# Kernel tuning notes

Hardware: AMD Instinct MI355X
Metric: run time of the kernel (lower is better)

The kernel has to match this reference:

```python
import jax, jax.numpy as jnp
import numpy as np

B = 1024      # batch
H = 512       # n_hidden
F = 32        # lstm_features
CIN = 4       # input channels
K = 30        # conv kernel
STRIDE = 6
L = 924       # input length -> T = (924-30)//6+1 = 150
KD = 40       # deconv kernel
NSTEPS = 10   # lstm_future_out
DN = ('NCH', 'OIH', 'NCH')


def setup_inputs() -> dict:
    key = jax.random.key(0)
    ks = jax.random.split(key, 14)
    s = 0.05
    rn = lambda k, shape: jax.random.normal(k, shape, jnp.float32) * s
    return dict(
        x=jax.random.normal(ks[0], (B, CIN, L), jnp.float32),
        conv_w=rn(ks[1], (F, CIN, K)), conv_b=rn(ks[2], (F,)),
        Wih0=rn(ks[3], (4 * H, F)), Whh0=rn(ks[4], (4 * H, H)),
        bih0=rn(ks[5], (4 * H,)), bhh0=rn(ks[6], (4 * H,)),
        Wih1=rn(ks[7], (4 * H, H)), Whh1=rn(ks[8], (4 * H, H)),
        bih1=rn(ks[9], (4 * H,)), bhh1=rn(ks[10], (4 * H,)),
        dec_w=rn(ks[11], (F, H)), dec_b=rn(ks[12], (F,)),
        deconv_w=rn(ks[13], (F, 1, KD)),
    )


def _cell(x, h, c, Wih, Whh, b):
    # PyTorch LSTM gate order: i, f, g, o
    g = x @ Wih.T + h @ Whh.T + b
    i, f, gg, o = jnp.split(g, 4, axis=-1)
    c = jax.nn.sigmoid(f) * c + jax.nn.sigmoid(i) * jnp.tanh(gg)
    h = jax.nn.sigmoid(o) * jnp.tanh(c)
    return h, c


def _lstm_layer(seq, Wih, Whh, b):
    # seq: [T, B, in] -> ys: [T, B, H], final (h, c)
    n = seq.shape[1]
    h0 = jnp.zeros((n, H), seq.dtype)
    c0 = jnp.zeros((n, H), seq.dtype)
    def step(carry, x):
        h, c = _cell(x, carry[0], carry[1], Wih, Whh, b)
        return (h, c), h
    (hT, cT), ys = jax.lax.scan(step, (h0, c0), seq)
    return ys, hT, cT


def _forward(x, conv_w, conv_b, Wih0, Whh0, bih0, bhh0,
             Wih1, Whh1, bih1, bhh1, dec_w, dec_b, deconv_w):
    # encoder conv: [B,4,L] -> [B,F,T]
    z = jax.lax.conv_general_dilated(x, conv_w, (STRIDE,), [(0, 0)],
                                     dimension_numbers=DN) + conv_b[None, :, None]
    z = jax.nn.relu(z)
    seq = jnp.transpose(z, (2, 0, 1))  # [T, B, F]
    b0, b1 = bih0 + bhh0, bih1 + bhh1
    s0, h0, c0 = _lstm_layer(seq, Wih0, Whh0, b0)
    s1, h1, c1 = _lstm_layer(s0, Wih1, Whh1, b1)
    out = s1 @ dec_w.T + dec_b                 # [T, B, F]
    y0 = out[-1]                               # output[-2:-1] of encoder -> last decoded step
    def dec_step(carry, _):
        y, ha, ca, hb, cb = carry
        ha, ca = _cell(y, ha, ca, Wih0, Whh0, b0)
        hb, cb = _cell(ha, hb, cb, Wih1, Whh1, b1)
        y = hb @ dec_w.T + dec_b
        return (y, ha, ca, hb, cb), y
    _, fut = jax.lax.scan(dec_step, (y0, h0, c0, h1, c1), None, length=NSTEPS)
    fut = jnp.transpose(fut, (1, 2, 0))        # [B, F, 10]
    # ConvTranspose1d (stride=1, pad=0, no bias) == cross-correlation with
    # spatially flipped, channel-swapped kernel on input padded by KD-1.
    kt = jnp.transpose(jnp.flip(deconv_w, -1), (1, 0, 2))  # [1, F, KD]
    return jax.lax.conv_general_dilated(fut, kt, (1,), [(KD - 1, KD - 1)],
                                        dimension_numbers=DN)  # [B, 1, 49]


def reference(x, conv_w, conv_b, Wih0, Whh0, bih0, bhh0,
              Wih1, Whh1, bih1, bhh1, dec_w, dec_b, deconv_w):
    return _forward(x, conv_w, conv_b, Wih0, Whh0, bih0, bhh0,
                    Wih1, Whh1, bih1, bhh1, dec_w, dec_b, deconv_w)
```

## Files before the change

### kernel.cpp

```cpp
#include <hip/hip_runtime.h>
#include <hip/hip_bf16.h>

typedef __hip_bfloat16 bf16;
typedef __attribute__((ext_vector_type(8))) short short8;
typedef __attribute__((ext_vector_type(4))) float float4v;

#define B_    1024
#define H_    512
#define G4H   2048
#define F_    32
#define CIN_  4
#define K_    30
#define STRIDE_ 6
#define L_    924
#define T_    150
#define KD_   40
#define NSTEPS_ 10
#define BH    (B_ * H_)
#define STRF  16

__device__ __forceinline__ float sigmoidf_(float x) { return 1.f / (1.f + __expf(-x)); }
__device__ __forceinline__ float tanhf_(float x)    { return 1.f - 2.f / (__expf(2.f * x) + 1.f); }
__device__ __forceinline__ float b2f_(short s) {
    return __uint_as_float(((unsigned)(unsigned short)s) << 16);
}
__device__ __forceinline__ unsigned short f2bu_(float v) {
    union { __hip_bfloat16 b; unsigned short u; } cv;
    cv.b = __float2bfloat16(v);
    return cv.u;
}
__device__ __forceinline__ void stwt_(bf16* p, float v) {
    __hip_atomic_store((unsigned short*)p, f2bu_(v), __ATOMIC_RELAXED, __HIP_MEMORY_SCOPE_AGENT);
}

__global__ __launch_bounds__(256) void cvt_kernel(const float* __restrict__ src,
                                                  bf16* __restrict__ dst, int n) {
    int i = blockIdx.x * 256 + threadIdx.x;
    if (i < n) dst[i] = __float2bfloat16(src[i]);
}

__global__ void bias_kernel(const float* __restrict__ bih0, const float* __restrict__ bhh0,
                            const float* __restrict__ bih1, const float* __restrict__ bhh1,
                            float* __restrict__ b0, float* __restrict__ b1) {
    int i = blockIdx.x * 256 + threadIdx.x;
    if (i < G4H)      b0[i] = bih0[i] + bhh0[i];
    else if (i < 2*G4H) { int j = i - G4H; b1[j] = bih1[j] + bhh1[j]; }
}

__global__ __launch_bounds__(256) void conv_kernel(
    const float* __restrict__ x, const float* __restrict__ w,
    const float* __restrict__ cb, bf16* __restrict__ seq)
{
    __shared__ float w_lds[CIN_ * K_ * F_];
    __shared__ float x_lds[CIN_ * L_];
    int tid = threadIdx.x;
    int b = blockIdx.x;
    for (int i = tid; i < CIN_ * K_ * F_; i += 256) {
        int f = i & 31, r = i >> 5;
        w_lds[r * 32 + f] = w[f * (CIN_ * K_) + r];
    }
    const float* xb = x + (size_t)b * (CIN_ * L_);
    for (int i = tid; i < CIN_ * L_; i += 256)
        x_lds[i] = xb[i];
    __syncthreads();
    int f = tid & 31, tt = tid >> 5;
    float cbf = cb[f];
    for (int t0 = 0; t0 < T_; t0 += 8) {
        int t = t0 + tt;
        if (t < T_) {
            float acc = cbf;
            #pragma unroll
            for (int c = 0; c < CIN_; ++c) {
                const float* xr = x_lds + c * L_ + t * STRIDE_;
                const float* wr = w_lds + c * K_ * 32 + f;
                #pragma unroll
                for (int k = 0; k < K_; ++k)
                    acc += xr[k] * wr[k * 32];
            }
            acc = fmaxf(acc, 0.f);
            seq[(size_t)t * (B_ * F_) + b * F_ + f] = __float2bfloat16(acc);
        }
    }
}

__device__ __forceinline__ void wait2(const int* fa, int ta, const int* fb, int tb) {
    const int t = threadIdx.x;
    if (t < 64) {
        const int* p = nullptr; int tgt = 0;
        if (t < 32) { if (fa) { p = fa + t * STRF;        tgt = ta; } }
        else        { if (fb) { p = fb + (t - 32) * STRF; tgt = tb; } }
        for (;;) {
            int v = p ? __hip_atomic_load(p, __ATOMIC_RELAXED, __HIP_MEMORY_SCOPE_AGENT)
                      : 0x7fffffff;
            if (__all(v >= tgt)) break;
            __builtin_amdgcn_s_sleep(2);
        }
    }
    __syncthreads();
    __builtin_amdgcn_fence(__ATOMIC_ACQUIRE, "agent");
}

__device__ __forceinline__ void signal1(int* f, int val) {
    __syncthreads();
    if (threadIdx.x == 0) {
        __builtin_amdgcn_s_waitcnt(0);
        __hip_atomic_store(f, val, __ATOMIC_RELAXED, __HIP_MEMORY_SCOPE_AGENT);
    }
}

template<int P1KS, int XSTR, typename MW>
__device__ __forceinline__ void layer_step(
    const bf16* __restrict__ X, const bf16* __restrict__ Hprev,
    const short8* __restrict__ WldsH, const short8* __restrict__ WldsI,
    float bi, float bff, float bg, float bo,
    float (&creg)[16], bf16* __restrict__ Hwt, bf16* __restrict__ Hloc,
    int m0, int j0, int wid, int lane, MW&& midwait)
{
    const int row16 = lane & 15;
    const int quad  = lane >> 4;
    const int mrow  = m0 + wid * 64 + row16;

    constexpr int TOT = 16 + P1KS;
    constexpr int NC  = (TOT + 3) / 4;

    const bf16* hb[4];
    const bf16* xb[4];
    #pragma unroll
    for (int q = 0; q < 4; ++q) {
        hb[q] = Hprev + (size_t)(mrow + q * 16) * H_ + quad * 8;
        xb[q] = X + (size_t)(mrow + q * 16) * XSTR + quad * 8;
    }

    float4v st[2][4][4];

    auto issue = [&](int c) {
        #pragma unroll
        for (int g = 0; g < 4; ++g) {
            int k = c * 4 + g;
            if (k < TOT) {
                #pragma unroll
                for (int q = 0; q < 4; ++q)
                    st[c & 1][g][q] = (k < 16)
                        ? *(const float4v*)(hb[q] + k * 32)
                        : *(const float4v*)(xb[q] + (k - 16) * 32);
            }
        }
        __builtin_amdgcn_sched_barrier(0);
    };
    auto ka = [&](int c) {
        #pragma unroll
        for (int g = 0; g < 4; ++g) {
            int k = c * 4 + g;
            if (k < TOT) {
                #pragma unroll
                for (int q = 0; q < 4; ++q)
                    asm volatile("" :: "v"(st[c & 1][g][q]));
            }
        }
    };

    issue(0);
    if (NC > 1) issue(1);
    midwait();

    float4v acc[4][4];
    #pragma unroll
    for (int q = 0; q < 4; ++q)
        #pragma unroll
        for (int g = 0; g < 4; ++g)
            acc[q][g] = (float4v){0.f, 0.f, 0.f, 0.f};

    #pragma unroll
    for (int c = 0; c < NC; ++c) {
        ka(c);
        #pragma unroll
        for (int g = 0; g < 4; ++g) {
            int k = c * 4 + g;
            if (k < TOT) {
                const short8* W = (k < 16) ? WldsH : WldsI;
                const int ks = (k < 16) ? k : (k - 16);
                short8 av[4];
                #pragma unroll
                for (int q = 0; q < 4; ++q)
                    av[q] = __builtin_bit_cast(short8, st[c & 1][g][q]);
                #pragma unroll
                for (int gg = 0; gg < 4; ++gg) {
                    short8 bfr = W[(ks * 4 + gg) * 64 + lane];
                    #pragma unroll
                    for (int q = 0; q < 4; ++q)
                        acc[q][gg] = __builtin_amdgcn_mfma_f32_16x16x32_bf16(av[q], bfr, acc[q][gg], 0, 0, 0);
                }
            }
        }
        if (c + 2 < NC) issue(c + 2);
    }

    float hval[16];
    #pragma unroll
    for (int ms = 0; ms < 4; ++ms) {
        #pragma unroll
        for (int r = 0; r < 4; ++r) {
            float ig = sigmoidf_(acc[ms][0][r] + bi);
            float fg = sigmoidf_(acc[ms][1][r] + bff);
            float gg = tanhf_(acc[ms][2][r] + bg);
            float og = sigmoidf_(acc[ms][3][r] + bo);
            float cn = fg * creg[ms * 4 + r] + ig * gg;
            creg[ms * 4 + r] = cn;
            hval[ms * 4 + r] = og * tanhf_(cn);
        }
    }

    unsigned wA[16];
    #pragma unroll
    for (int i = 0; i < 16; ++i) {
        float o = __shfl_xor(hval[i], 1);
        float lo = (lane & 1) ? o : hval[i];
        float hi = (lane & 1) ? hval[i] : o;
        wA[i] = (unsigned)f2bu_(lo) | ((unsigned)f2bu_(hi) << 16);
    }
    unsigned long long q[16];
    #pragma unroll
    for (int i = 0; i < 16; ++i) {
        unsigned o2 = __shfl_xor(wA[i], 2);
        q[i] = (lane & 2) ? (((unsigned long long)wA[i] << 32) | o2)
                          : (((unsigned long long)o2 << 32) | wA[i]);
    }
    const int cchunk = j0 + (row16 & ~3);
    #pragma unroll
    for (int i = 0; i < 16; ++i) {
        if ((i >> 2) == (lane & 3)) {
            int ms = i >> 2, r = i & 3;
            size_t off = (size_t)(m0 + wid * 64 + ms * 16 + quad * 4 + r) * H_ + cchunk;
            if (Hwt)
                __hip_atomic_store((unsigned long long*)(Hwt + off), q[i],
                                   __ATOMIC_RELAXED, __HIP_MEMORY_SCOPE_AGENT);
            if (Hloc)
                *(unsigned long long*)(Hloc + off) = q[i];
        }
    }
}

struct PP {
    const bf16 *seq, *Wih0, *Whh0, *Wih1, *Whh1, *dwb;
    const float *b0, *b1, *dec_b;
    float *fut;
    bf16 *h0, *h0loc, *h1, *y;
    int *flags;
};

__global__ __launch_bounds__(256, 1) void lstm_persist(PP P) {
    __shared__ short8 WldsH[4096];
    __shared__ short8 WldsI[4096];

    const int bid   = blockIdx.x;
    const int gsw   = bid & 7;
    const bool isL0 = (gsw < 4);
    const int mg    = gsw & 3;
    const int jj    = bid >> 3;
    const int lb    = mg * 32 + jj;
    const int j0    = jj * 16;
    const int m0    = mg * 256;
    const int tid   = threadIdx.x;
    const int wid   = tid >> 6;
    const int lane  = tid & 63;

    {
        const bf16* Whh = isL0 ? P.Whh0 : P.Whh1;
        for (int i = 0; i < 16; ++i) {
            int s = tid + i * 256;
            int frag = s >> 6, ln = s & 63;
            int ks = frag >> 2, g = frag & 3;
            WldsH[s] = *(const short8*)(Whh + (size_t)(g * H_ + j0 + (ln & 15)) * H_
                                        + ks * 32 + (ln >> 4) * 8);
        }
        if (isL0) {
            int frag = tid >> 6, ln = tid & 63;
            int g = frag & 3;
            WldsI[tid] = *(const short8*)(P.Wih0 + (size_t)(g * H_ + j0 + (ln & 15)) * F_
                                          + (ln >> 4) * 8);
        } else {
            for (int i = 0; i < 16; ++i) {
                int s = tid + i * 256;
                int frag = s >> 6, ln = s & 63;
                int ks = frag >> 2, g = frag & 3;
                WldsI[s] = *(const short8*)(P.Wih1 + (size_t)(g * H_ + j0 + (ln & 15)) * H_
                                            + ks * 32 + (ln >> 4) * 8);
            }
        }
        __syncthreads();
    }

    const float* bias = isL0 ? P.b0 : P.b1;
    const int jb  = j0 + (lane & 15);
    const float bi  = bias[jb];
    const float bff = bias[H_ + jb];
    const float bg  = bias[2 * H_ + jb];
    const float bo  = bias[3 * H_ + jb];

    float creg[16];
    #pragma unroll
    for (int i = 0; i < 16; ++i) creg[i] = 0.f;

    int* f0 = P.flags;
    int* f1 = P.flags + 128 * STRF;
    int* fy = P.flags + 256 * STRF;
    const int* f0g = f0 + mg * 32 * STRF;
    const int* f1g = f1 + mg * 32 * STRF;
    const int* fyg = fy + mg * 32 * STRF;

    auto noop = []{};

    if (isL0) {
        for (int t = 0; t < T_; ++t) {
            wait2(f0g, t, f1g, t - 2);
            layer_step<1, 32>(P.seq + (size_t)t * B_ * F_,
                              P.h0loc + (size_t)((t + 2) % 3) * BH, WldsH, WldsI,
                              bi, bff, bg, bo, creg,
                              P.h0 + (size_t)(t % 3) * BH,
                              P.h0loc + (size_t)(t % 3) * BH,
                              m0, j0, wid, lane, noop);
            signal1(f0 + lb * STRF, t + 1);
        }
        for (int s = 0; s <= NSTEPS_; ++s) {
            wait2(f1g, T_ + s, (s >= 1) ? f0g : nullptr, T_ + s);
            {
                int id = lb * 256 + tid;
                int br = id >> 5, f = id & 31;
                const short8* hv = (const short8*)(P.h1 + (size_t)((T_ - 1 + s) % 3) * BH
                                                   + (size_t)br * H_);
                const short8* wv = (const short8*)(P.dwb + (size_t)f * H_);
                float acc = P.dec_b[f];
                for (int i = 0; i < H_ / 8; ++i) {
                    short8 h8 = hv[i], w8 = wv[i];
                    #pragma unroll
                    for (int k = 0; k < 8; ++k)
                        acc += b2f_(h8[k]) * b2f_(w8[k]);
                }
                stwt_(P.y + id, acc);
                if (s >= 1)
                    P.fut[(size_t)br * (F_ * NSTEPS_) + f * NSTEPS_ + (s - 1)] = acc;
            }
            signal1(fy + lb * STRF, s + 1);
            if (s < NSTEPS_) {
                int t = T_ + s;
                wait2(f0g, t, f1g, t - 2);
                wait2(fyg, s + 1, nullptr, 0);
                layer_step<1, 32>(P.y,
                                  P.h0loc + (size_t)((t + 2) % 3) * BH, WldsH, WldsI,
                                  bi, bff, bg, bo, creg,
                                  P.h0 + (size_t)(t % 3) * BH,
                                  P.h0loc + (size_t)(t % 3) * BH,
                                  m0, j0, wid, lane, noop);
                signal1(f0 + lb * STRF, t + 1);
            }
        }
    } else {
        for (int t = 0; t < T_ + NSTEPS_; ++t) {
            wait2(f1g, t, nullptr, 0);
            bf16* hout = P.h1 + (size_t)(t % 3) * BH;
            bool wt = (t >= T_ - 1);
            layer_step<16, 512>(P.h0 + (size_t)(t % 3) * BH,
                                P.h1 + (size_t)((t + 2) % 3) * BH, WldsH, WldsI,
                                bi, bff, bg, bo, creg,
                                wt ? hout : nullptr,
                                wt ? nullptr : hout,
                                m0, j0, wid, lane,
                                [&]{ wait2(f0g, t + 1, nullptr, 0); });
            signal1(f1 + lb * STRF, t + 1);
        }
    }
}

__global__ __launch_bounds__(256) void deconv_kernel(
    const float* __restrict__ fut, const float* __restrict__ dw,
    float* __restrict__ out)
{
    int idx = blockIdx.x * 256 + threadIdx.x;
    if (idx >= B_ * 49) return;
    int b = idx / 49, jj = idx % 49;
    int tlo = jj - (KD_ - 1); if (tlo < 0) tlo = 0;
    int thi = jj; if (thi > NSTEPS_ - 1) thi = NSTEPS_ - 1;
    float acc = 0.f;
    for (int f = 0; f < F_; ++f) {
        const float* fr = fut + (size_t)b * (F_ * NSTEPS_) + f * NSTEPS_;
        const float* wr = dw + f * KD_;
        for (int t = tlo; t <= thi; ++t)
            acc += fr[t] * wr[jj - t];
    }
    out[idx] = acc;
}

extern "C" void kernel_launch(void* const* d_in, const int* in_sizes, int n_in,
                              void* d_out, int out_size, void* d_ws, size_t ws_size,
                              hipStream_t stream) {
    const float* x       = (const float*)d_in[0];
    const float* conv_w  = (const float*)d_in[1];
    const float* conv_b  = (const float*)d_in[2];
    const float* Wih0f   = (const float*)d_in[3];
    const float* Whh0f   = (const float*)d_in[4];
    const float* bih0    = (const float*)d_in[5];
    const float* bhh0    = (const float*)d_in[6];
    const float* Wih1f   = (const float*)d_in[7];
    const float* Whh1f   = (const float*)d_in[8];
    const float* bih1    = (const float*)d_in[9];
    const float* bhh1    = (const float*)d_in[10];
    const float* dec_wf  = (const float*)d_in[11];
    const float* dec_b   = (const float*)d_in[12];
    const float* deconvw = (const float*)d_in[13];
    float* out = (float*)d_out;

    char* ws = (char*)d_ws;
    size_t off = 0;
    auto alloc = [&](size_t bytes) { char* p = ws + off; off = (off + bytes + 255) & ~(size_t)255; return p; };
    bf16*  seq   = (bf16*) alloc((size_t)T_ * B_ * F_ * 2);
    float* b0v   = (float*)alloc(G4H * 4);
    float* b1v   = (float*)alloc(G4H * 4);
    bf16*  h0    = (bf16*) alloc((size_t)3 * BH * 2);
    bf16*  h0loc = (bf16*) alloc((size_t)3 * BH * 2);
    bf16*  h1    = (bf16*) alloc((size_t)3 * BH * 2);
    bf16*  y     = (bf16*) alloc((size_t)B_ * F_ * 2);
    float* fut   = (float*)alloc((size_t)B_ * F_ * NSTEPS_ * 4);
    bf16*  Wih0b = (bf16*) alloc((size_t)G4H * F_ * 2);
    bf16*  Whh0b = (bf16*) alloc((size_t)G4H * H_ * 2);
    bf16*  Wih1b = (bf16*) alloc((size_t)G4H * H_ * 2);
    bf16*  Whh1b = (bf16*) alloc((size_t)G4H * H_ * 2);
    bf16*  dec_wb= (bf16*) alloc((size_t)F_ * H_ * 2);
    int*   flags = (int*)  alloc(3 * 128 * STRF * 4);

    hipMemsetAsync(h0, 0, (size_t)3 * BH * 2, stream);
    hipMemsetAsync(h0loc, 0, (size_t)3 * BH * 2, stream);
    hipMemsetAsync(h1, 0, (size_t)3 * BH * 2, stream);
    hipMemsetAsync(flags, 0, 3 * 128 * STRF * 4, stream);

    cvt_kernel<<<(G4H * F_ + 255) / 256, 256, 0, stream>>>(Wih0f, Wih0b, G4H * F_);
    cvt_kernel<<<(G4H * H_ + 255) / 256, 256, 0, stream>>>(Whh0f, Whh0b, G4H * H_);
    cvt_kernel<<<(G4H * H_ + 255) / 256, 256, 0, stream>>>(Wih1f, Wih1b, G4H * H_);
    cvt_kernel<<<(G4H * H_ + 255) / 256, 256, 0, stream>>>(Whh1f, Whh1b, G4H * H_);
    cvt_kernel<<<(F_ * H_ + 255) / 256, 256, 0, stream>>>(dec_wf, dec_wb, F_ * H_);

    bias_kernel<<<16, 256, 0, stream>>>(bih0, bhh0, bih1, bhh1, b0v, b1v);
    conv_kernel<<<B_, 256, 0, stream>>>(x, conv_w, conv_b, seq);

    PP P;
    P.seq = seq; P.Wih0 = Wih0b; P.Whh0 = Whh0b; P.Wih1 = Wih1b; P.Whh1 = Whh1b;
    P.dwb = dec_wb; P.b0 = b0v; P.b1 = b1v; P.dec_b = dec_b;
    P.fut = fut; P.h0 = h0; P.h0loc = h0loc; P.h1 = h1; P.y = y;
    P.flags = flags;

    void* args[] = { &P };
    hipError_t err = hipLaunchCooperativeKernel((const void*)lstm_persist,
                                                dim3(256), dim3(256), args, 0, stream);
    if (err != hipSuccess) {
        lstm_persist<<<256, 256, 0, stream>>>(P);
    }

    deconv_kernel<<<196, 256, 0, stream>>>(fut, deconvw, out);
}
```

Before: 6.000 ms.

## Replace acquire fence with device-scope atomic loads of shared hidden states

Drops the separate local copy of layer-0 hidden state (h0loc) and the plain/atomic dual store path, so every hidden-state write is one device-scope relaxed atomic store. Reads of cross-block data (h, y, decoder input) become relaxed atomic 8-byte loads, and the agent-scope acquire fence after each wait is removed. The aim is to avoid the cache invalidation cost of the acquire fence and the duplicate writes on every timestep. It relies on relaxed atomics to bypass stale cache lines, which may be slower per load and weakens the ordering guarantees.

Measured after the change: 6.040 ms. Within noise of the previous version (+0.7%).

```diff
diff --git a/kernel.cpp b/kernel.cpp
--- a/kernel.cpp
+++ b/kernel.cpp
@@ -31,6 +31,13 @@
 }
 __device__ __forceinline__ void stwt_(bf16* p, float v) {
     __hip_atomic_store((unsigned short*)p, f2bu_(v), __ATOMIC_RELAXED, __HIP_MEMORY_SCOPE_AGENT);
+}
+__device__ __forceinline__ float4v ldbp16_(const bf16* p) {
+    const unsigned long long* q = (const unsigned long long*)p;
+    union { unsigned long long u[2]; float4v v; } cv;
+    cv.u[0] = __hip_atomic_load(q,     __ATOMIC_RELAXED, __HIP_MEMORY_SCOPE_AGENT);
+    cv.u[1] = __hip_atomic_load(q + 1, __ATOMIC_RELAXED, __HIP_MEMORY_SCOPE_AGENT);
+    return cv.v;
 }
 
 __global__ __launch_bounds__(256) void cvt_kernel(const float* __restrict__ src,
@@ -97,7 +104,6 @@
         }
     }
     __syncthreads();
-    __builtin_amdgcn_fence(__ATOMIC_ACQUIRE, "agent");
 }
 
 __device__ __forceinline__ void signal1(int* f, int val) {
@@ -108,12 +114,12 @@
     }
 }
 
-template<int P1KS, int XSTR, typename MW>
+template<int P1KS, int XSTR, bool XBP, typename MW>
 __device__ __forceinline__ void layer_step(
     const bf16* __restrict__ X, const bf16* __restrict__ Hprev,
     const short8* __restrict__ WldsH, const short8* __restrict__ WldsI,
     float bi, float bff, float bg, float bo,
-    float (&creg)[16], bf16* __restrict__ Hwt, bf16* __restrict__ Hloc,
+    float (&creg)[16], bf16* __restrict__ Hout,
     int m0, int j0, int wid, int lane, MW&& midwait)
 {
     const int row16 = lane & 15;
@@ -139,10 +145,14 @@
             int k = c * 4 + g;
             if (k < TOT) {
                 #pragma unroll
-                for (int q = 0; q < 4; ++q)
-                    st[c & 1][g][q] = (k < 16)
-                        ? *(const float4v*)(hb[q] + k * 32)
-                        : *(const float4v*)(xb[q] + (k - 16) * 32);
+                for (int q = 0; q < 4; ++q) {
+                    if (k < 16)
+                        st[c & 1][g][q] = ldbp16_(hb[q] + k * 32);
+                    else if (XBP)
+                        st[c & 1][g][q] = ldbp16_(xb[q] + (k - 16) * 32);
+                    else
+                        st[c & 1][g][q] = *(const float4v*)(xb[q] + (k - 16) * 32);
+                }
             }
         }
         __builtin_amdgcn_sched_barrier(0);
@@ -231,11 +241,8 @@
         if ((i >> 2) == (lane & 3)) {
             int ms = i >> 2, r = i & 3;
             size_t off = (size_t)(m0 + wid * 64 + ms * 16 + quad * 4 + r) * H_ + cchunk;
-            if (Hwt)
-                __hip_atomic_store((unsigned long long*)(Hwt + off), q[i],
-                                   __ATOMIC_RELAXED, __HIP_MEMORY_SCOPE_AGENT);
-            if (Hloc)
-                *(unsigned long long*)(Hloc + off) = q[i];
+            __hip_atomic_store((unsigned long long*)(Hout + off), q[i],
+                               __ATOMIC_RELAXED, __HIP_MEMORY_SCOPE_AGENT);
         }
     }
 }
@@ -244,7 +251,7 @@
     const bf16 *seq, *Wih0, *Whh0, *Wih1, *Whh1, *dwb;
     const float *b0, *b1, *dec_b;
     float *fut;
-    bf16 *h0, *h0loc, *h1, *y;
+    bf16 *h0, *h1, *y;
     int *flags;
 };
 
@@ -313,11 +320,10 @@
     if (isL0) {
         for (int t = 0; t < T_; ++t) {
             wait2(f0g, t, f1g, t - 2);
-            layer_step<1, 32>(P.seq + (size_t)t * B_ * F_,
-                              P.h0loc + (size_t)((t + 2) % 3) * BH, WldsH, WldsI,
+            layer_step<1, 32, false>(P.seq + (size_t)t * B_ * F_,
+                              P.h0 + (size_t)((t + 2) % 3) * BH, WldsH, WldsI,
                               bi, bff, bg, bo, creg,
                               P.h0 + (size_t)(t % 3) * BH,
-                              P.h0loc + (size_t)(t % 3) * BH,
                               m0, j0, wid, lane, noop);
             signal1(f0 + lb * STRF, t + 1);
         }
@@ -326,12 +332,16 @@
             {
                 int id = lb * 256 + tid;
                 int br = id >> 5, f = id & 31;
-                const short8* hv = (const short8*)(P.h1 + (size_t)((T_ - 1 + s) % 3) * BH
-                                                   + (size_t)br * H_);
+                const unsigned long long* hq =
+                    (const unsigned long long*)(P.h1 + (size_t)((T_ - 1 + s) % 3) * BH
+                                                + (size_t)br * H_);
                 const short8* wv = (const short8*)(P.dwb + (size_t)f * H_);
                 float acc = P.dec_b[f];
                 for (int i = 0; i < H_ / 8; ++i) {
-                    short8 h8 = hv[i], w8 = wv[i];
+                    union { unsigned long long u[2]; short8 s; } hh;
+                    hh.u[0] = __hip_atomic_load(hq + 2 * i,     __ATOMIC_RELAXED, __HIP_MEMORY_SCOPE_AGENT);
+                    hh.u[1] = __hip_atomic_load(hq + 2 * i + 1, __ATOMIC_RELAXED, __HIP_MEMORY_SCOPE_AGENT);
+                    short8 h8 = hh.s, w8 = wv[i];
                     #pragma unroll
                     for (int k = 0; k < 8; ++k)
                         acc += b2f_(h8[k]) * b2f_(w8[k]);
@@ -345,11 +355,10 @@
                 int t = T_ + s;
                 wait2(f0g, t, f1g, t - 2);
                 wait2(fyg, s + 1, nullptr, 0);
-                layer_step<1, 32>(P.y,
-                                  P.h0loc + (size_t)((t + 2) % 3) * BH, WldsH, WldsI,
+                layer_step<1, 32, true>(P.y,
+                                  P.h0 + (size_t)((t + 2) % 3) * BH, WldsH, WldsI,
                                   bi, bff, bg, bo, creg,
                                   P.h0 + (size_t)(t % 3) * BH,
-                                  P.h0loc + (size_t)(t % 3) * BH,
                                   m0, j0, wid, lane, noop);
                 signal1(f0 + lb * STRF, t + 1);
             }
@@ -357,13 +366,10 @@
     } else {
         for (int t = 0; t < T_ + NSTEPS_; ++t) {
             wait2(f1g, t, nullptr, 0);
-            bf16* hout = P.h1 + (size_t)(t % 3) * BH;
-            bool wt = (t >= T_ - 1);
-            layer_step<16, 512>(P.h0 + (size_t)(t % 3) * BH,
+            layer_step<16, 512, true>(P.h0 + (size_t)(t % 3) * BH,
                                 P.h1 + (size_t)((t + 2) % 3) * BH, WldsH, WldsI,
                                 bi, bff, bg, bo, creg,
-                                wt ? hout : nullptr,
-                                wt ? nullptr : hout,
+                                P.h1 + (size_t)(t % 3) * BH,
                                 m0, j0, wid, lane,
                                 [&]{ wait2(f0g, t + 1, nullptr, 0); });
             signal1(f1 + lb * STRF, t + 1);
@@ -416,7 +422,6 @@
     float* b0v   = (float*)alloc(G4H * 4);
     float* b1v   = (float*)alloc(G4H * 4);
     bf16*  h0    = (bf16*) alloc((size_t)3 * BH * 2);
-    bf16*  h0loc = (bf16*) alloc((size_t)3 * BH * 2);
     bf16*  h1    = (bf16*) alloc((size_t)3 * BH * 2);
     bf16*  y     = (bf16*) alloc((size_t)B_ * F_ * 2);
     float* fut   = (float*)alloc((size_t)B_ * F_ * NSTEPS_ * 4);
@@ -428,7 +433,6 @@
     int*   flags = (int*)  alloc(3 * 128 * STRF * 4);
 
     hipMemsetAsync(h0, 0, (size_t)3 * BH * 2, stream);
-    hipMemsetAsync(h0loc, 0, (size_t)3 * BH * 2, stream);
     hipMemsetAsync(h1, 0, (size_t)3 * BH * 2, stream);
     hipMemsetAsync(flags, 0, 3 * 128 * STRF * 4, stream);
 
@@ -444,7 +448,7 @@
     PP P;
     P.seq = seq; P.Wih0 = Wih0b; P.Whh0 = Whh0b; P.Wih1 = Wih1b; P.Whh1 = Whh1b;
     P.dwb = dec_wb; P.b0 = b0v; P.b1 = b1v; P.dec_b = dec_b;
-    P.fut = fut; P.h0 = h0; P.h0loc = h0loc; P.h1 = h1; P.y = y;
+    P.fut = fut; P.h0 = h0; P.h1 = h1; P.y = y;
     P.flags = flags;
 
     void* args[] = { &P };
```
